# Kernel optimization log

Measured on AMD Instinct MI355X. Metric: run time of the kernel, lower is better.

Reference implementation:

```python
import jax, jax.numpy as jnp
import numpy as np

N_NODES = 100000
N_EDGES = 1280000
IN_DIM = 64
HID = 64
OUT_DIM = 2
N_GRAPHS = 1000
BN_EPS = 1e-5


def setup_inputs() -> dict:
    key = jax.random.key(0)
    ks = jax.random.split(key, 16)
    x = jax.random.normal(ks[0], (N_NODES, IN_DIM), dtype=jnp.float32)
    edge_index = jax.random.randint(ks[1], (2, N_EDGES), 0, N_NODES, dtype=jnp.int64)
    batch = jnp.sort(jax.random.randint(ks[2], (N_NODES,), 0, N_GRAPHS, dtype=jnp.int64))
    # He-init linear weights (stored as [in, out] so forward is x @ W)
    def he(k, fan_in, fan_out):
        return jax.random.normal(k, (fan_in, fan_out), dtype=jnp.float32) * np.sqrt(2.0 / fan_in)
    return {
        "x": x,
        "edge_index": edge_index,
        "batch": batch,
        "bn_in_g": jnp.ones((IN_DIM,), jnp.float32),
        "bn_in_b": jnp.zeros((IN_DIM,), jnp.float32),
        "W1": he(ks[3], IN_DIM, HID), "b1": jnp.zeros((HID,), jnp.float32),
        "g1": jnp.ones((HID,), jnp.float32), "be1": jnp.zeros((HID,), jnp.float32),
        "W2": he(ks[4], HID, HID), "b2": jnp.zeros((HID,), jnp.float32),
        "g2": jnp.ones((HID,), jnp.float32), "be2": jnp.zeros((HID,), jnp.float32),
        "Wout": he(ks[5], HID, OUT_DIM), "bout": jnp.zeros((OUT_DIM,), jnp.float32),
    }


def _batchnorm(x, g, b):
    # training-mode BN over the node dimension (biased variance, as torch uses for normalization)
    m = jnp.mean(x, axis=0)
    v = jnp.mean(jnp.square(x - m), axis=0)
    return (x - m) * jax.lax.rsqrt(v + BN_EPS) * g + b


def _gcn_norm(edge_index, n):
    # PyG GCNConv normalization with added self-loops:
    # norm_e = deg[src]^-1/2 * deg[dst]^-1/2, deg computed on A + I over targets.
    row = jnp.concatenate([edge_index[0], jnp.arange(n, dtype=edge_index.dtype)])
    col = jnp.concatenate([edge_index[1], jnp.arange(n, dtype=edge_index.dtype)])
    deg = jax.ops.segment_sum(jnp.ones_like(col, dtype=jnp.float32), col, num_segments=n)
    dinv = jnp.where(deg > 0, jax.lax.rsqrt(deg), 0.0)
    norm = dinv[row] * dinv[col]
    return row, col, norm


def _gcn_conv(x, W, b, row, col, norm, n):
    h = x @ W                                   # [N, out]
    msg = h[row] * norm[:, None]                # gather over edges (incl. self-loops)
    agg = jax.ops.segment_sum(msg, col, num_segments=n)
    return agg + b


def reference(x, edge_index, batch, bn_in_g, bn_in_b, W1, b1, g1, be1, W2, b2, g2, be2, Wout, bout):
    n = x.shape[0]
    row, col, norm = _gcn_norm(edge_index, n)
    h = _batchnorm(x, bn_in_g, bn_in_b)         # input BN (dropout = identity in eval)
    h = _gcn_conv(h, W1, b1, row, col, norm, n)
    h = _batchnorm(jax.nn.relu(h), g1, be1)
    h = _gcn_conv(h, W2, b2, row, col, norm, n)
    h = _batchnorm(jax.nn.relu(h), g2, be2)
    # global mean pool per graph
    sums = jax.ops.segment_sum(h, batch, num_segments=N_GRAPHS)
    cnts = jax.ops.segment_sum(jnp.ones((n,), h.dtype), batch, num_segments=N_GRAPHS)
    pooled = sums / jnp.maximum(cnts, 1.0)[:, None]
    return pooled @ Wout + bout                 # [N_GRAPHS, OUT_DIM]
```

## Files before the change

### kernel.cpp

```cpp
#include <hip/hip_runtime.h>
#include <math.h>

#define N_NODES 100000
#define N_EDGES 1280000
#define DIM 64
#define N_GRAPHS 1000
#define BN_EPS 1e-5f
#define NB 392
#define P1B 256
#define P1E 5000
#define SB 400
#define WIN 128
#define NWIN (N_EDGES / WIN)
#define NSLOT 32

__device__ __forceinline__ unsigned int bf16_rtn2(float a, float b) {
    unsigned int ua = __float_as_uint(a);
    unsigned int ub = __float_as_uint(b);
    ua = (ua + 0x7FFFu + ((ua >> 16) & 1u)) >> 16;
    ub = (ub + 0x7FFFu + ((ub >> 16) & 1u)) >> 16;
    return ua | (ub << 16);
}
__device__ __forceinline__ unsigned short bf16r(float a) {
    unsigned int u = __float_as_uint(a);
    return (unsigned short)((u + 0x7FFFu + ((u >> 16) & 1u)) >> 16);
}
__device__ __forceinline__ float bfup(unsigned short u) {
    return __uint_as_float(((unsigned int)u) << 16);
}
__device__ __forceinline__ float blo(unsigned int v) { return __uint_as_float(v << 16); }
__device__ __forceinline__ float bhi(unsigned int v) { return __uint_as_float(v & 0xFFFF0000u); }

__global__ __launch_bounds__(256) void k_p1hist(const int* __restrict__ ei,
                                                const int* __restrict__ batch,
                                                const float* __restrict__ X,
                                                int* __restrict__ bh,
                                                int* __restrict__ start,
                                                float* __restrict__ gs400,
                                                float* __restrict__ gq400) {
    int t = threadIdx.x;
    if (blockIdx.x < P1B) {
        __shared__ int hist[NB];
        for (int b = t; b < NB; b += 256) hist[b] = 0;
        __syncthreads();
        int e0 = blockIdx.x * P1E;
        #pragma unroll 4
        for (int e = e0 + t; e < e0 + P1E; e += 256)
            atomicAdd(&hist[ei[N_EDGES + e] >> 8], 1);
        __syncthreads();
        for (int b = t; b < NB; b += 256) bh[b * P1B + blockIdx.x] = hist[b];
    } else if (blockIdx.x < P1B + SB) {
        int grp = blockIdx.x - P1B;
        int j = t & 63, rg = t >> 6;
        int base = grp * 250;
        float s = 0.f, s2 = 0.f;
        for (int i = base + rg; i < base + 250; i += 4) {
            float v = X[i * DIM + j];
            s += v; s2 += v * v;
        }
        __shared__ float ls[256], ls2[256];
        ls[t] = s; ls2[t] = s2;
        __syncthreads();
        if (t < 64) {
            s  = ls[j]  + ls[64 + j]  + ls[128 + j]  + ls[192 + j];
            s2 = ls2[j] + ls2[64 + j] + ls2[128 + j] + ls2[192 + j];
            gs400[grp * DIM + j] = s;
            gq400[grp * DIM + j] = s2;
        }
    } else {
        int i = (blockIdx.x - P1B - SB) * 256 + t;
        if (i < N_NODES) {
            int cur = batch[i];
            if (i == 0) { for (int q = 0; q <= cur; q++) start[q] = 0; }
            else {
                int prev = batch[i - 1];
                for (int q = prev + 1; q <= cur; q++) start[q] = i;
            }
            if (i == N_NODES - 1)
                for (int q = cur + 1; q <= N_GRAPHS; q++) start[q] = N_NODES;
        }
    }
}

__global__ __launch_bounds__(256) void k_scan1(const int* __restrict__ bh,
                                               int* __restrict__ iscan,
                                               int* __restrict__ bsum,
                                               const float* __restrict__ gs400,
                                               const float* __restrict__ gq400,
                                               const float* __restrict__ bng,
                                               const float* __restrict__ bnb,
                                               const float* __restrict__ W1,
                                               float* __restrict__ Wsc,
                                               float* __restrict__ cshift,
                                               float* __restrict__ gsum32) {
    int t = threadIdx.x;
    if (blockIdx.x == NB) {
        __shared__ float ssc[64], shl[64];
        if (t < 64) {
            float ms = 0.f, m2 = 0.f;
            for (int k2 = 0; k2 < SB; k2++) {
                ms += gs400[k2 * DIM + t];
                m2 += gq400[k2 * DIM + t];
            }
            float mean = ms * (1.0f / N_NODES);
            float var  = m2 * (1.0f / N_NODES) - mean * mean;
            float inv  = 1.0f / sqrtf(var + BN_EPS);
            float sc   = bng[t] * inv;
            ssc[t] = sc;
            shl[t] = bnb[t] - mean * sc;
        }
        __syncthreads();
        if (t < 64) {
            float s = 0.f;
            for (int k2 = 0; k2 < DIM; k2++) s += shl[k2] * W1[k2 * DIM + t];
            cshift[t] = s;
        }
        for (int z = t; z < 4096; z += 256) Wsc[z] = W1[z] * ssc[z >> 6];
        for (int z = t; z < 2 * NSLOT * DIM; z += 256) gsum32[z] = 0.f;
        return;
    }
    __shared__ int ls[256];
    int i = blockIdx.x * 256 + t;
    int v = bh[i];
    ls[t] = v;
    __syncthreads();
    for (int off = 1; off < 256; off <<= 1) {
        int tv = (t >= off) ? ls[t - off] : 0;
        __syncthreads();
        ls[t] += tv;
        __syncthreads();
    }
    iscan[i] = ls[t];
    if (t == 255) bsum[blockIdx.x] = ls[255];
}

__global__ __launch_bounds__(256) void k_p1scat(const int* __restrict__ ei,
                                                const int* __restrict__ bh,
                                                const int* __restrict__ iscan,
                                                const int* __restrict__ bsum,
                                                int* __restrict__ tmp) {
    __shared__ int cur[NB];
    __shared__ int s0[256], s1[256];
    int t = threadIdx.x, blk = blockIdx.x;
    int v0 = bsum[t];
    int v1 = (t < NB - 256) ? bsum[256 + t] : 0;
    s0[t] = v0; s1[t] = v1;
    __syncthreads();
    for (int off = 1; off < 256; off <<= 1) {
        int a0 = (t >= off) ? s0[t - off] : 0;
        int a1 = (t >= off) ? s1[t - off] : 0;
        __syncthreads();
        s0[t] += a0; s1[t] += a1;
        __syncthreads();
    }
    int carry = s0[255];
    {
        int i = t * P1B + blk;
        cur[t] = (s0[t] - v0) + iscan[i] - bh[i];
    }
    if (t < NB - 256) {
        int b = 256 + t;
        int i = b * P1B + blk;
        cur[b] = (carry + s1[t] - v1) + iscan[i] - bh[i];
    }
    __syncthreads();
    int e0 = blk * P1E;
    for (int e = e0 + t; e < e0 + P1E; e += 256) {
        int r = ei[e], c = ei[N_EDGES + e];
        int pos = atomicAdd(&cur[c >> 8], 1);
        tmp[pos] = (r << 8) | (c & 255);
    }
}

__global__ __launch_bounds__(256) void k_p2(const int* __restrict__ tmp,
                                            const int* __restrict__ bsum,
                                            int* __restrict__ rowstart,
                                            float* __restrict__ dinv,
                                            int* __restrict__ winnode,
                                            float* __restrict__ C,
                                            int* __restrict__ csr) {
    int b = blockIdx.x, t = threadIdx.x;
    __shared__ int red[256];
    int part = 0;
    for (int k2 = t; k2 < b; k2 += 256) part += bsum[k2];
    red[t] = part;
    __syncthreads();
    for (int off = 128; off; off >>= 1) {
        if (t < off) red[t] += red[t + off];
        __syncthreads();
    }
    int bstart = red[0];
    int bend = bstart + bsum[b];
    __shared__ int cnt[256], scn[256], curs[256];
    cnt[t] = 0;
    __syncthreads();
    for (int e = bstart + t; e < bend; e += 256)
        atomicAdd(&cnt[tmp[e] & 255], 1);
    __syncthreads();
    scn[t] = cnt[t];
    __syncthreads();
    for (int off = 1; off < 256; off <<= 1) {
        int v = (t >= off) ? scn[t - off] : 0;
        __syncthreads();
        scn[t] += v;
        __syncthreads();
    }
    int node = b * 256 + t;
    int deg = cnt[t];
    int rs = bstart + scn[t] - deg;
    bool span = false;
    if (node <= N_NODES) rowstart[node] = rs;
    if (node == N_NODES) rowstart[node + 1] = rs;
    if (node < N_NODES) {
        dinv[node] = 1.0f / sqrtf((float)(deg + 1));
        int re = rs + deg;
        for (int w = (rs + WIN - 1) / WIN; w * WIN < re; ++w) winnode[w] = node;
        span = (deg > 0) && (rs / WIN != (re - 1) / WIN);
    }
    int lane = t & 63;
    int wbase = b * 256 + (t & ~63);
    unsigned long long m = __ballot(span);
    while (m) {
        int bit = __builtin_ctzll(m);
        m &= m - 1;
        C[(size_t)(wbase + bit) * DIM + lane] = 0.f;
    }
    curs[t] = rs;
    __syncthreads();
    for (int e = bstart + t; e < bend; e += 256) {
        int rec = tmp[e];
        int pos = atomicAdd(&curs[rec & 255], 1);
        csr[pos] = (int)((unsigned)rec >> 8);
    }
}

__global__ void k_bnfold(float* __restrict__ gsum, float* __restrict__ gsumsq,
                         const float* __restrict__ g, const float* __restrict__ b,
                         const float* __restrict__ W,
                         float* __restrict__ Wsc, float* __restrict__ cshift) {
    int j = threadIdx.x;
    float ms = 0.f, m2 = 0.f;
    for (int k = 0; k < NSLOT; k++) {
        ms += gsum[k * DIM + j];   gsum[k * DIM + j] = 0.f;
        m2 += gsumsq[k * DIM + j]; gsumsq[k * DIM + j] = 0.f;
    }
    float mean = ms * (1.0f / N_NODES);
    float var  = m2 * (1.0f / N_NODES) - mean * mean;
    float inv  = 1.0f / sqrtf(var + BN_EPS);
    float sc   = g[j] * inv;
    __shared__ float ssc[64], shl[64];
    ssc[j] = sc;
    shl[j] = b[j] - mean * sc;
    __syncthreads();
    float s = 0.f;
    for (int k = 0; k < DIM; k++) s += shl[k] * W[k * DIM + j];
    cshift[j] = s;
    for (int z = j; z < 4096; z += 64) Wsc[z] = W[z] * ssc[z >> 6];
}

__global__ __launch_bounds__(256) void k_gemm_f32(const float* __restrict__ X,
                                                  const float* __restrict__ Wsc,
                                                  const float* __restrict__ cshift,
                                                  const float* __restrict__ dinv,
                                                  unsigned short* __restrict__ T) {
    __shared__ float Al[64 * 65];
    int row0 = blockIdx.x * 64;
    for (int t = threadIdx.x; t < 4096; t += 256) {
        int r = t >> 6, k = t & 63;
        int i = row0 + r;
        Al[r * 65 + k] = (i < N_NODES) ? X[(size_t)i * DIM + k] : 0.f;
    }
    __syncthreads();
    int r = threadIdx.x & 63;
    int qu = __builtin_amdgcn_readfirstlane(threadIdx.x >> 6);
    float acc[16];
    #pragma unroll
    for (int jj = 0; jj < 16; jj++) acc[jj] = cshift[qu * 16 + jj];
    #pragma unroll 4
    for (int k = 0; k < 64; k++) {
        float a = Al[r * 65 + k];
        const float4* wv = (const float4*)(Wsc + (k << 6) + (qu << 4));
        float4 w0 = wv[0], w1 = wv[1], w2 = wv[2], w3 = wv[3];
        acc[0]  += a * w0.x; acc[1]  += a * w0.y; acc[2]  += a * w0.z; acc[3]  += a * w0.w;
        acc[4]  += a * w1.x; acc[5]  += a * w1.y; acc[6]  += a * w1.z; acc[7]  += a * w1.w;
        acc[8]  += a * w2.x; acc[9]  += a * w2.y; acc[10] += a * w2.z; acc[11] += a * w2.w;
        acc[12] += a * w3.x; acc[13] += a * w3.y; acc[14] += a * w3.z; acc[15] += a * w3.w;
    }
    int i = row0 + r;
    if (i < N_NODES) {
        float dv = dinv[i];
        unsigned int pk[8];
        #pragma unroll
        for (int jj = 0; jj < 8; jj++)
            pk[jj] = bf16_rtn2(acc[2 * jj] * dv, acc[2 * jj + 1] * dv);
        uint4* outv = (uint4*)&T[(size_t)i * DIM + qu * 16];
        outv[0] = make_uint4(pk[0], pk[1], pk[2], pk[3]);
        outv[1] = make_uint4(pk[4], pk[5], pk[6], pk[7]);
    }
}

__global__ __launch_bounds__(256) void k_gemm_b16(const unsigned short* __restrict__ X,
                                                  const float* __restrict__ Wsc,
                                                  const float* __restrict__ cshift,
                                                  const float* __restrict__ dinv,
                                                  unsigned short* __restrict__ T,
                                                  float* __restrict__ pool) {
    if (blockIdx.x < N_GRAPHS && threadIdx.x < 64)
        pool[(size_t)blockIdx.x * DIM + threadIdx.x] = 0.f;
    __shared__ float Al[64 * 65];
    int row0 = blockIdx.x * 64;
    for (int t = threadIdx.x; t < 4096; t += 256) {
        int r = t >> 6, k = t & 63;
        int i = row0 + r;
        Al[r * 65 + k] = (i < N_NODES) ? bfup(X[(size_t)i * DIM + k]) : 0.f;
    }
    __syncthreads();
    int r = threadIdx.x & 63;
    int qu = __builtin_amdgcn_readfirstlane(threadIdx.x >> 6);
    float acc[16];
    #pragma unroll
    for (int jj = 0; jj < 16; jj++) acc[jj] = cshift[qu * 16 + jj];
    #pragma unroll 4
    for (int k = 0; k < 64; k++) {
        float a = Al[r * 65 + k];
        const float4* wv = (const float4*)(Wsc + (k << 6) + (qu << 4));
        float4 w0 = wv[0], w1 = wv[1], w2 = wv[2], w3 = wv[3];
        acc[0]  += a * w0.x; acc[1]  += a * w0.y; acc[2]  += a * w0.z; acc[3]  += a * w0.w;
        acc[4]  += a * w1.x; acc[5]  += a * w1.y; acc[6]  += a * w1.z; acc[7]  += a * w1.w;
        acc[8]  += a * w2.x; acc[9]  += a * w2.y; acc[10] += a * w2.z; acc[11] += a * w2.w;
        acc[12] += a * w3.x; acc[13] += a * w3.y; acc[14] += a * w3.z; acc[15] += a * w3.w;
    }
    int i = row0 + r;
    if (i < N_NODES) {
        float dv = dinv[i];
        unsigned int pk[8];
        #pragma unroll
        for (int jj = 0; jj < 8; jj++)
            pk[jj] = bf16_rtn2(acc[2 * jj] * dv, acc[2 * jj + 1] * dv);
        uint4* outv = (uint4*)&T[(size_t)i * DIM + qu * 16];
        outv[0] = make_uint4(pk[0], pk[1], pk[2], pk[3]);
        outv[1] = make_uint4(pk[4], pk[5], pk[6], pk[7]);
    }
}

#define SWZ(V, S) __builtin_amdgcn_ds_swizzle((V), (((S) << 5) | 0x10))

#define ISSUE(SRCV, TVV, CV, S0) do {                                 \
    SRCV[0] = SWZ(CV, (S0) + 0); SRCV[1] = SWZ(CV, (S0) + 1);         \
    SRCV[2] = SWZ(CV, (S0) + 2); SRCV[3] = SWZ(CV, (S0) + 3);         \
    TVV[0] = T2[(unsigned)SRCV[0] * 16u + cc];                        \
    TVV[1] = T2[(unsigned)SRCV[1] * 16u + cc];                        \
    TVV[2] = T2[(unsigned)SRCV[2] * 16u + cc];                        \
    TVV[3] = T2[(unsigned)SRCV[3] * 16u + cc];                        \
} while (0)

#define STEP(TVV, U, B, FL) do {                                      \
    const int ebs = e0 + 16 * (B) + 4 * (U);                          \
    uint2 tvv = TVV[U];                                               \
    float a0 = blo(tvv.x), a1 = bhi(tvv.x);                           \
    float a2 = blo(tvv.y), a3 = bhi(tvv.y);                           \
    if (re > ebs + 3) {                                               \
        acc0 += a0; acc1 += a1; acc2 += a2; acc3 += a3;               \
    } else {                                                          \
        int lo = ebs;                                                 \
        while (re <= ebs + 3) {                                       \
            int eg = ebs + gg;                                        \
            if (eg >= lo && eg < re) {                                \
                acc0 += a0; acc1 += a1; acc2 += a2; acc3 += a3;       \
            }                                                         \
            lo = re;                                                  \
            FL();                                                     \
        }                                                             \
        if (ebs + gg >= lo) {                                         \
            acc0 += a0; acc1 += a1; acc2 += a2; acc3 += a3;           \
        }                                                             \
    }                                                                 \
} while (0)

#define CONSUME(TVV, B, FL) do {                                      \
    STEP(TVV, 0, B, FL); STEP(TVV, 1, B, FL);                         \
    STEP(TVV, 2, B, FL); STEP(TVV, 3, B, FL);                         \
} while (0)

#define COMB4()                                                       \
    float t0 = acc0 + __shfl_xor(acc0, 16); t0 += __shfl_xor(t0, 32); \
    float t1 = acc1 + __shfl_xor(acc1, 16); t1 += __shfl_xor(t1, 32); \
    float t2 = acc2 + __shfl_xor(acc2, 16); t2 += __shfl_xor(t2, 32); \
    float t3 = acc3 + __shfl_xor(acc3, 16); t3 += __shfl_xor(t3, 32);

#define REDIST64(OUT, V0, V1, V2, V3)                                 \
    float _r0 = __shfl((V0), lane >> 2);                              \
    float _r1 = __shfl((V1), lane >> 2);                              \
    float _r2 = __shfl((V2), lane >> 2);                              \
    float _r3 = __shfl((V3), lane >> 2);                              \
    float OUT = (lane & 2) ? ((lane & 1) ? _r3 : _r2)                 \
                           : ((lane & 1) ? _r1 : _r0);

#define ADVANCE() do {                                                \
    acc0 = acc1 = acc2 = acc3 = 0.f;                                  \
    ++i; ++k;                                                         \
    if (k < 64) re = __builtin_amdgcn_readlane(rsv, k);               \
    else        re = __builtin_amdgcn_readfirstlane(rowstart[i + 1]); \
    tsv = T2[(unsigned)i * 16u + cc];                                 \
} while (0)

#define FLUSH1() do {                                                 \
    COMB4();                                                          \
    if (part) {                                                       \
        REDIST64(cv, t0, t1, t2, t3);                                 \
        atomicAdd(&C[(size_t)i * DIM + lane], cv);                    \
        part = false;                                                 \
    } else {                                                          \
        int cnt = i - i0;                                             \
        float di;                                                     \
        if (cnt < 64)                                                 \
            di = __int_as_float(                                      \
                __builtin_amdgcn_readlane(__float_as_int(dv), cnt));  \
        else di = dinv[i];                                            \
        float h0 = fmaxf((t0 + blo(tsv.x)) * di + bb.x, 0.f);         \
        float h1 = fmaxf((t1 + bhi(tsv.x)) * di + bb.y, 0.f);         \
        float h2 = fmaxf((t2 + blo(tsv.y)) * di + bb.z, 0.f);         \
        float h3 = fmaxf((t3 + bhi(tsv.y)) * di + bb.w, 0.f);         \
        if (lane < 16)                                                \
            ((uint2*)H)[(unsigned)i * 16u + cc] =                     \
                make_uint2(bf16_rtn2(h0, h1), bf16_rtn2(h2, h3));     \
        s0 += h0; s1 += h1; s2 += h2; s3 += h3;                       \
        q0 += h0 * h0; q1 += h1 * h1; q2 += h2 * h2; q3 += h3 * h3;   \
    }                                                                 \
    ADVANCE();                                                        \
} while (0)

__global__ __launch_bounds__(256) void k_gather1(const unsigned short* __restrict__ T,
                                                 const float* __restrict__ dinv,
                                                 const int* __restrict__ rowstart,
                                                 const int* __restrict__ winnode,
                                                 const int* __restrict__ csr,
                                                 const float* __restrict__ bias,
                                                 float* __restrict__ C,
                                                 unsigned short* __restrict__ H,
                                                 float* __restrict__ gsum,
                                                 float* __restrict__ gsumsq) {
    const int lane = threadIdx.x & 63;
    const int gg = lane >> 4;
    const int cc = lane & 15;
    const int w = blockIdx.x * 4 + (threadIdx.x >> 6);
    const int e0 = w * WIN;
    const int eend = e0 + WIN;
    const uint2* T2 = (const uint2*)T;

    int csrv0 = csr[e0 + 4 * cc + gg];
    int csrv1 = csr[e0 + 64 + 4 * cc + gg];
    int i0 = __builtin_amdgcn_readfirstlane(winnode[w]);
    int rsv = rowstart[min(i0 + lane, N_NODES + 1)];
    float dv = dinv[min(i0 + lane, N_NODES - 1)];
    uint2 tsv = T2[(unsigned)i0 * 16u + cc];
    const float4 bb = ((const float4*)bias)[cc];

    int i = i0, k = 1;
    int re = __builtin_amdgcn_readlane(rsv, 1);
    bool part = __builtin_amdgcn_readlane(rsv, 0) < e0;
    float acc0 = 0.f, acc1 = 0.f, acc2 = 0.f, acc3 = 0.f;
    float s0 = 0.f, s1 = 0.f, s2 = 0.f, s3 = 0.f;
    float q0 = 0.f, q1 = 0.f, q2 = 0.f, q3 = 0.f;

    int srcA[4], srcB[4], srcC[4], srcD[4];
    uint2 tva[4], tvb[4], tvc[4], tvd[4];
    ISSUE(srcA, tva, csrv0, 0);
    ISSUE(srcB, tvb, csrv0, 4);
    ISSUE(srcC, tvc, csrv0, 8);
    ISSUE(srcD, tvd, csrv0, 12);
    CONSUME(tva, 0, FLUSH1);  ISSUE(srcA, tva, csrv1, 0);
    CONSUME(tvb, 1, FLUSH1);  ISSUE(srcB, tvb, csrv1, 4);
    CONSUME(tvc, 2, FLUSH1);  ISSUE(srcC, tvc, csrv1, 8);
    CONSUME(tvd, 3, FLUSH1);  ISSUE(srcD, tvd, csrv1, 12);
    CONSUME(tva, 4, FLUSH1);
    CONSUME(tvb, 5, FLUSH1);
    CONSUME(tvc, 6, FLUSH1);
    CONSUME(tvd, 7, FLUSH1);

    if (part || re > eend) {
        COMB4();
        REDIST64(cv, t0, t1, t2, t3);
        atomicAdd(&C[(size_t)i * DIM + lane], cv);
    } else {
        FLUSH1();
    }

    __shared__ float shs[4][64], shq[4][64];
    int wv = threadIdx.x >> 6;
    if (lane < 16) {
        shs[wv][4 * cc + 0] = s0; shs[wv][4 * cc + 1] = s1;
        shs[wv][4 * cc + 2] = s2; shs[wv][4 * cc + 3] = s3;
        shq[wv][4 * cc + 0] = q0; shq[wv][4 * cc + 1] = q1;
        shq[wv][4 * cc + 2] = q2; shq[wv][4 * cc + 3] = q3;
    }
    __syncthreads();
    if (threadIdx.x < 64) {
        int j = threadIdx.x;
        float vs = shs[0][j] + shs[1][j] + shs[2][j] + shs[3][j];
        float vq = shq[0][j] + shq[1][j] + shq[2][j] + shq[3][j];
        int slot = (blockIdx.x & (NSLOT - 1)) * DIM;
        atomicAdd(&gsum[slot + j], vs);
        atomicAdd(&gsumsq[slot + j], vq);
    }
}

#define FLUSH2() do {                                                 \
    COMB4();                                                          \
    if (part) {                                                       \
        REDIST64(cv, t0, t1, t2, t3);                                 \
        atomicAdd(&C[(size_t)i * DIM + lane], cv);                    \
        part = false;                                                 \
    } else {                                                          \
        int cnt = i - i0;                                             \
        float di;                                                     \
        int gi;                                                       \
        if (cnt < 64) {                                               \
            di = __int_as_float(                                      \
                __builtin_amdgcn_readlane(__float_as_int(dv), cnt));  \
            gi = __builtin_amdgcn_readlane(bv, cnt);                  \
        } else { di = dinv[i]; gi = batch[i]; }                       \
        float h0 = fmaxf((t0 + blo(tsv.x)) * di + bb.x, 0.f);         \
        float h1 = fmaxf((t1 + bhi(tsv.x)) * di + bb.y, 0.f);         \
        float h2 = fmaxf((t2 + blo(tsv.y)) * di + bb.z, 0.f);         \
        float h3 = fmaxf((t3 + bhi(tsv.y)) * di + bb.w, 0.f);         \
        s0 += h0; s1 += h1; s2 += h2; s3 += h3;                       \
        q0 += h0 * h0; q1 += h1 * h1; q2 += h2 * h2; q3 += h3 * h3;   \
        if (gi != cur_g) {                                            \
            if (cur_g >= 0) {                                         \
                REDIST64(pv, ps0, ps1, ps2, ps3);                     \
                atomicAdd(&pool[(size_t)cur_g * DIM + lane], pv);     \
            }                                                         \
            ps0 = ps1 = ps2 = ps3 = 0.f;                              \
            cur_g = gi;                                               \
        }                                                             \
        ps0 += h0; ps1 += h1; ps2 += h2; ps3 += h3;                   \
    }                                                                 \
    ADVANCE();                                                        \
} while (0)

__global__ __launch_bounds__(256) void k_gather2(const unsigned short* __restrict__ T,
                                                 const float* __restrict__ dinv,
                                                 const int* __restrict__ rowstart,
                                                 const int* __restrict__ winnode,
                                                 const int* __restrict__ csr,
                                                 const float* __restrict__ bias,
                                                 const int* __restrict__ batch,
                                                 float* __restrict__ C,
                                                 float* __restrict__ pool,
                                                 float* __restrict__ gsum,
                                                 float* __restrict__ gsumsq) {
    const int lane = threadIdx.x & 63;
    const int gg = lane >> 4;
    const int cc = lane & 15;
    const int w = blockIdx.x * 4 + (threadIdx.x >> 6);
    const int e0 = w * WIN;
    const int eend = e0 + WIN;
    const uint2* T2 = (const uint2*)T;

    int csrv0 = csr[e0 + 4 * cc + gg];
    int csrv1 = csr[e0 + 64 + 4 * cc + gg];
    int i0 = __builtin_amdgcn_readfirstlane(winnode[w]);
    int rsv = rowstart[min(i0 + lane, N_NODES + 1)];
    float dv = dinv[min(i0 + lane, N_NODES - 1)];
    int bv = batch[min(i0 + lane, N_NODES - 1)];
    uint2 tsv = T2[(unsigned)i0 * 16u + cc];
    const float4 bb = ((const float4*)bias)[cc];

    int i = i0, k = 1;
    int re = __builtin_amdgcn_readlane(rsv, 1);
    bool part = __builtin_amdgcn_readlane(rsv, 0) < e0;
    float acc0 = 0.f, acc1 = 0.f, acc2 = 0.f, acc3 = 0.f;
    float s0 = 0.f, s1 = 0.f, s2 = 0.f, s3 = 0.f;
    float q0 = 0.f, q1 = 0.f, q2 = 0.f, q3 = 0.f;
    float ps0 = 0.f, ps1 = 0.f, ps2 = 0.f, ps3 = 0.f;
    int cur_g = -1;

    int srcA[4], srcB[4], srcC[4], srcD[4];
    uint2 tva[4], tvb[4], tvc[4], tvd[4];
    ISSUE(srcA, tva, csrv0, 0);
    ISSUE(srcB, tvb, csrv0, 4);
    ISSUE(srcC, tvc, csrv0, 8);
    ISSUE(srcD, tvd, csrv0, 12);
    CONSUME(tva, 0, FLUSH2);  ISSUE(srcA, tva, csrv1, 0);
    CONSUME(tvb, 1, FLUSH2);  ISSUE(srcB, tvb, csrv1, 4);
    CONSUME(tvc, 2, FLUSH2);  ISSUE(srcC, tvc, csrv1, 8);
    CONSUME(tvd, 3, FLUSH2);  ISSUE(srcD, tvd, csrv1, 12);
    CONSUME(tva, 4, FLUSH2);
    CONSUME(tvb, 5, FLUSH2);
    CONSUME(tvc, 6, FLUSH2);
    CONSUME(tvd, 7, FLUSH2);

    if (part || re > eend) {
        COMB4();
        REDIST64(cv, t0, t1, t2, t3);
        atomicAdd(&C[(size_t)i * DIM + lane], cv);
    } else {
        FLUSH2();
    }
    if (cur_g >= 0) {
        REDIST64(pv, ps0, ps1, ps2, ps3);
        atomicAdd(&pool[(size_t)cur_g * DIM + lane], pv);
    }

    __shared__ float shs[4][64], shq[4][64];
    int wv = threadIdx.x >> 6;
    if (lane < 16) {
        shs[wv][4 * cc + 0] = s0; shs[wv][4 * cc + 1] = s1;
        shs[wv][4 * cc + 2] = s2; shs[wv][4 * cc + 3] = s3;
        shq[wv][4 * cc + 0] = q0; shq[wv][4 * cc + 1] = q1;
        shq[wv][4 * cc + 2] = q2; shq[wv][4 * cc + 3] = q3;
    }
    __syncthreads();
    if (threadIdx.x < 64) {
        int j = threadIdx.x;
        float vs = shs[0][j] + shs[1][j] + shs[2][j] + shs[3][j];
        float vq = shq[0][j] + shq[1][j] + shq[2][j] + shq[3][j];
        int slot = (blockIdx.x & (NSLOT - 1)) * DIM;
        atomicAdd(&gsum[slot + j], vs);
        atomicAdd(&gsumsq[slot + j], vq);
    }
}

__global__ __launch_bounds__(256) void k_strad1(float* __restrict__ C,
                                                const unsigned short* __restrict__ T,
                                                const float* __restrict__ dinv,
                                                const int* __restrict__ rowstart,
                                                const int* __restrict__ winnode,
                                                const float* __restrict__ bias,
                                                unsigned short* __restrict__ H,
                                                float* __restrict__ gsum,
                                                float* __restrict__ gsumsq) {
    int lane = threadIdx.x & 63;
    int wv = threadIdx.x >> 6;
    float bb = bias[lane];
    float s = 0.f, s2 = 0.f;
    __shared__ int anyw;
    if (threadIdx.x == 0) anyw = 0;
    __syncthreads();
    if (blockIdx.x < NWIN / 4) {
        int w = blockIdx.x * 4 + wv;
        int n = winnode[w];
        int rs = rowstart[n];
        if (w == rs / WIN + 1) {
            float di = dinv[n];
            float c = C[(size_t)n * DIM + lane];
            C[(size_t)n * DIM + lane] = 0.f;
            float h = fmaxf((c + bfup(T[(size_t)n * DIM + lane])) * di + bb, 0.f);
            H[(size_t)n * DIM + lane] = bf16r(h);
            s += h; s2 += h * h;
            anyw = 1;
        }
    } else {
        int base = (blockIdx.x - NWIN / 4) * 256 + wv * 64;
        int nb = base + lane;
        int d0 = 0;
        if (nb < N_NODES)
            d0 = (rowstart[nb + 1] == rowstart[nb]) && ((rowstart[nb] & (WIN - 1)) == 0);
        unsigned long long m = __ballot(d0);
        while (m) {
            int b = __builtin_ctzll(m);
            m &= m - 1;
            int n = base + b;
            float di = dinv[n];
            float h = fmaxf(bfup(T[(size_t)n * DIM + lane]) * di + bb, 0.f);
            H[(size_t)n * DIM + lane] = bf16r(h);
            s += h; s2 += h * h;
            anyw = 1;
        }
    }
    __shared__ float ls[256], ls2[256];
    ls[threadIdx.x] = s; ls2[threadIdx.x] = s2;
    __syncthreads();
    if (anyw && threadIdx.x < 64) {
        int j = threadIdx.x;
        int slot = (blockIdx.x & (NSLOT - 1)) * DIM;
        atomicAdd(&gsum[slot + j],   ls[j] + ls[64 + j] + ls[128 + j] + ls[192 + j]);
        atomicAdd(&gsumsq[slot + j], ls2[j] + ls2[64 + j] + ls2[128 + j] + ls2[192 + j]);
    }
}

__global__ __launch_bounds__(256) void k_strad2(const float* __restrict__ C,
                                                const unsigned short* __restrict__ T,
                                                const float* __restrict__ dinv,
                                                const int* __restrict__ rowstart,
                                                const int* __restrict__ winnode,
                                                const float* __restrict__ bias,
                                                const int* __restrict__ batch,
                                                float* __restrict__ pool,
                                                float* __restrict__ gsum,
                                                float* __restrict__ gsumsq) {
    int lane = threadIdx.x & 63;
    int wv = threadIdx.x >> 6;
    float bb = bias[lane];
    float s = 0.f, s2 = 0.f;
    __shared__ int anyw;
    if (threadIdx.x == 0) anyw = 0;
    __syncthreads();
    if (blockIdx.x < NWIN / 4) {
        int w = blockIdx.x * 4 + wv;
        int n = winnode[w];
        int rs = rowstart[n];
        if (w == rs / WIN + 1) {
            float di = dinv[n];
            float h = fmaxf((C[(size_t)n * DIM + lane]
                             + bfup(T[(size_t)n * DIM + lane])) * di + bb, 0.f);
            s += h; s2 += h * h;
            atomicAdd(&pool[(size_t)batch[n] * DIM + lane], h);
            anyw = 1;
        }
    } else {
        int base = (blockIdx.x - NWIN / 4) * 256 + wv * 64;
        int nb = base + lane;
        int d0 = 0;
        if (nb < N_NODES)
            d0 = (rowstart[nb + 1] == rowstart[nb]) && ((rowstart[nb] & (WIN - 1)) == 0);
        unsigned long long m = __ballot(d0);
        while (m) {
            int b = __builtin_ctzll(m);
            m &= m - 1;
            int n = base + b;
            float di = dinv[n];
            float h = fmaxf(bfup(T[(size_t)n * DIM + lane]) * di + bb, 0.f);
            s += h; s2 += h * h;
            atomicAdd(&pool[(size_t)batch[n] * DIM + lane], h);
            anyw = 1;
        }
    }
    __shared__ float ls[256], ls2[256];
    ls[threadIdx.x] = s; ls2[threadIdx.x] = s2;
    __syncthreads();
    if (anyw && threadIdx.x < 64) {
        int j = threadIdx.x;
        int slot = (blockIdx.x & (NSLOT - 1)) * DIM;
        atomicAdd(&gsum[slot + j],   ls[j] + ls[64 + j] + ls[128 + j] + ls[192 + j]);
        atomicAdd(&gsumsq[slot + j], ls2[j] + ls2[64 + j] + ls2[128 + j] + ls2[192 + j]);
    }
}

__global__ void k_final(const float* __restrict__ pool, const int* __restrict__ start,
                        const float* __restrict__ gsum, const float* __restrict__ gsumsq,
                        const float* __restrict__ g, const float* __restrict__ be,
                        const float* __restrict__ Wout, const float* __restrict__ bout,
                        float* __restrict__ out) {
    int gr = blockIdx.x;
    int l = threadIdx.x;
    float ms = 0.f, m2 = 0.f;
    for (int k = 0; k < NSLOT; k++) { ms += gsum[k * DIM + l]; m2 += gsumsq[k * DIM + l]; }
    float mean = ms * (1.0f / N_NODES);
    float var  = m2 * (1.0f / N_NODES) - mean * mean;
    float inv  = 1.0f / sqrtf(var + BN_EPS);
    float sc   = g[l] * inv;
    float sh   = be[l] - mean * sc;
    float c = fmaxf((float)(start[gr + 1] - start[gr]), 1.f);
    float p = (pool[gr * DIM + l] / c) * sc + sh;
    float a0 = p * Wout[l * 2 + 0];
    float a1 = p * Wout[l * 2 + 1];
    #pragma unroll
    for (int off = 32; off; off >>= 1) {
        a0 += __shfl_down(a0, off, 64);
        a1 += __shfl_down(a1, off, 64);
    }
    if (l == 0) {
        out[gr * 2 + 0] = a0 + bout[0];
        out[gr * 2 + 1] = a1 + bout[1];
    }
}

extern "C" void kernel_launch(void* const* d_in, const int* in_sizes, int n_in,
                              void* d_out, int out_size, void* d_ws, size_t ws_size,
                              hipStream_t stream) {
    (void)in_sizes; (void)n_in; (void)out_size; (void)ws_size;
    const float* x       = (const float*)d_in[0];
    const int*   ei      = (const int*)d_in[1];
    const int*   batch   = (const int*)d_in[2];
    const float* bn_in_g = (const float*)d_in[3];
    const float* bn_in_b = (const float*)d_in[4];
    const float* W1      = (const float*)d_in[5];
    const float* b1      = (const float*)d_in[6];
    const float* g1      = (const float*)d_in[7];
    const float* be1     = (const float*)d_in[8];
    const float* W2      = (const float*)d_in[9];
    const float* b2      = (const float*)d_in[10];
    const float* g2      = (const float*)d_in[11];
    const float* be2     = (const float*)d_in[12];
    const float* Wout    = (const float*)d_in[13];
    const float* bout    = (const float*)d_in[14];
    float* out = (float*)d_out;

    char* p = (char*)d_ws;
    float* C = (float*)p;                   p += (size_t)N_NODES * DIM * 4;
    unsigned short* H = (unsigned short*)p; p += (size_t)N_NODES * DIM * 2;
    unsigned short* T = (unsigned short*)p; p += (size_t)N_NODES * DIM * 2;
    int* csr = (int*)p;                     p += (size_t)N_EDGES * 4;
    float* dinv = (float*)p;                p += N_NODES * 4;
    int* bh = (int*)p;                      p += NB * P1B * 4;
    int* iscan = (int*)p;                   p += NB * P1B * 4;
    int* rowstart = (int*)p;                p += (N_NODES + 4) * 4;
    int* winnode = (int*)p;                 p += NWIN * 4;
    int* bsum = (int*)p;                    p += NB * 4;
    int* start = (int*)p;                   p += (N_GRAPHS + 4) * 4;
    float* gsum32 = (float*)p;              p += NSLOT * DIM * 4;
    float* gsumsq32 = (float*)p;            p += NSLOT * DIM * 4;
    float* gs400 = (float*)p;               p += (size_t)SB * DIM * 4;
    float* gq400 = (float*)p;               p += (size_t)SB * DIM * 4;
    float* Wsc = (float*)p;                 p += 4096 * 4;
    float* cshift = (float*)p;              p += DIM * 4;
    float* pool = (float*)p;                p += (size_t)N_GRAPHS * DIM * 4;
    int* tmp = (int*)H;

    k_p1hist<<<P1B + SB + 392, 256, 0, stream>>>(ei, batch, x, bh, start, gs400, gq400);
    k_scan1<<<NB + 1, 256, 0, stream>>>(bh, iscan, bsum, gs400, gq400,
                                        bn_in_g, bn_in_b, W1, Wsc, cshift, gsum32);
    k_p1scat<<<P1B, 256, 0, stream>>>(ei, bh, iscan, bsum, tmp);
    k_p2<<<NB, 256, 0, stream>>>(tmp, bsum, rowstart, dinv, winnode, C, csr);

    k_gemm_f32<<<(N_NODES + 63) / 64, 256, 0, stream>>>(x, Wsc, cshift, dinv, T);
    k_gather1<<<NWIN / 4, 256, 0, stream>>>(T, dinv, rowstart, winnode, csr, b1,
                                            C, H, gsum32, gsumsq32);
    k_strad1<<<NWIN / 4 + 392, 256, 0, stream>>>(C, T, dinv, rowstart, winnode, b1,
                                                 H, gsum32, gsumsq32);

    k_bnfold<<<1, 64, 0, stream>>>(gsum32, gsumsq32, g1, be1, W2, Wsc, cshift);
    k_gemm_b16<<<(N_NODES + 63) / 64, 256, 0, stream>>>(H, Wsc, cshift, dinv, T, pool);
    k_gather2<<<NWIN / 4, 256, 0, stream>>>(T, dinv, rowstart, winnode, csr, b2,
                                            batch, C, pool, gsum32, gsumsq32);
    k_strad2<<<NWIN / 4 + 392, 256, 0, stream>>>(C, T, dinv, rowstart, winnode, b2,
                                                 batch, pool, gsum32, gsumsq32);

    k_final<<<N_GRAPHS, 64, 0, stream>>>(pool, start, gsum32, gsumsq32, g2, be2,
                                         Wout, bout, out);
}
```

Before: 304.7 us.

## Stage edge bucketing in LDS and write contiguous runs per bucket

After: 339.4 us. 1.11x slower.

```diff
diff --git a/kernel.cpp b/kernel.cpp
--- a/kernel.cpp
+++ b/kernel.cpp
@@ -95,13 +95,19 @@
                                                float* __restrict__ gsum32) {
     int t = threadIdx.x;
     if (blockIdx.x == NB) {
+        __shared__ float red[256], red2[256];
         __shared__ float ssc[64], shl[64];
+        int j = t & 63, rg = t >> 6;
+        float ms = 0.f, m2 = 0.f;
+        for (int k2 = rg; k2 < SB; k2 += 4) {
+            ms += gs400[k2 * DIM + j];
+            m2 += gq400[k2 * DIM + j];
+        }
+        red[t] = ms; red2[t] = m2;
+        __syncthreads();
         if (t < 64) {
-            float ms = 0.f, m2 = 0.f;
-            for (int k2 = 0; k2 < SB; k2++) {
-                ms += gs400[k2 * DIM + t];
-                m2 += gq400[k2 * DIM + t];
-            }
+            ms = red[j] + red[64 + j] + red[128 + j] + red[192 + j];
+            m2 = red2[j] + red2[64 + j] + red2[128 + j] + red2[192 + j];
             float mean = ms * (1.0f / N_NODES);
             float var  = m2 * (1.0f / N_NODES) - mean * mean;
             float inv  = 1.0f / sqrtf(var + BN_EPS);
@@ -140,35 +146,63 @@
                                                 const int* __restrict__ bsum,
                                                 int* __restrict__ tmp) {
     __shared__ int cur[NB];
-    __shared__ int s0[256], s1[256];
+    __shared__ int lpre[NB];
+    __shared__ int lins[NB];
+    __shared__ int slds[P1E];
+    __shared__ int s0[256], s1[256], l0[256], l1[256];
     int t = threadIdx.x, blk = blockIdx.x;
     int v0 = bsum[t];
     int v1 = (t < NB - 256) ? bsum[256 + t] : 0;
-    s0[t] = v0; s1[t] = v1;
+    int i0x = t * P1B + blk;
+    int bh0 = bh[i0x];
+    int is0 = iscan[i0x];
+    int bh1 = 0, is1 = 0;
+    if (t < NB - 256) {
+        int i1x = (256 + t) * P1B + blk;
+        bh1 = bh[i1x];
+        is1 = iscan[i1x];
+    }
+    s0[t] = v0; s1[t] = v1; l0[t] = bh0; l1[t] = bh1;
     __syncthreads();
     for (int off = 1; off < 256; off <<= 1) {
         int a0 = (t >= off) ? s0[t - off] : 0;
         int a1 = (t >= off) ? s1[t - off] : 0;
-        __syncthreads();
-        s0[t] += a0; s1[t] += a1;
+        int b0 = (t >= off) ? l0[t - off] : 0;
+        int b1 = (t >= off) ? l1[t - off] : 0;
+        __syncthreads();
+        s0[t] += a0; s1[t] += a1; l0[t] += b0; l1[t] += b1;
         __syncthreads();
     }
     int carry = s0[255];
+    int lcarry = l0[255];
     {
-        int i = t * P1B + blk;
-        cur[t] = (s0[t] - v0) + iscan[i] - bh[i];
+        cur[t]  = (s0[t] - v0) + is0 - bh0;
+        int lp  = l0[t] - bh0;
+        lpre[t] = lp;
+        lins[t] = lp;
     }
     if (t < NB - 256) {
         int b = 256 + t;
-        int i = b * P1B + blk;
-        cur[b] = (carry + s1[t] - v1) + iscan[i] - bh[i];
+        cur[b]  = (carry + s1[t] - v1) + is1 - bh1;
+        int lp  = lcarry + l1[t] - bh1;
+        lpre[b] = lp;
+        lins[b] = lp;
     }
     __syncthreads();
     int e0 = blk * P1E;
     for (int e = e0 + t; e < e0 + P1E; e += 256) {
         int r = ei[e], c = ei[N_EDGES + e];
-        int pos = atomicAdd(&cur[c >> 8], 1);
-        tmp[pos] = (r << 8) | (c & 255);
+        int p = atomicAdd(&lins[c >> 8], 1);
+        slds[p] = (r << 8) | (c & 255);
+    }
+    __syncthreads();
+    int lane = t & 63, wv = t >> 6;
+    for (int b = wv; b < NB; b += 4) {
+        int base = cur[b];
+        int lp = lpre[b];
+        int len = ((b == NB - 1) ? P1E : lpre[b + 1]) - lp;
+        for (int l = lane; l < len; l += 64)
+            tmp[base + l] = slds[lp + l];
     }
 }
 
```
